# Performance work log

Hardware: AMD Instinct MI355X
Metric: run time of the kernel (lower is better)

The kernel has to match this reference:

```python
import jax, jax.numpy as jnp
import numpy as np

TAU = 2.0  # self.temperature
EPS = 1e-7

def setup_inputs() -> dict:
    key = jax.random.key(0)
    k1, k2, k3, k4, k5, k6 = jax.random.split(key, 6)
    B, S, H = 8, 4096, 512
    G, V, Dg = 2, 320, 128  # groups, codevectors per group, codevector_dim // G
    hidden_states = jax.random.normal(k1, (B, S, H), dtype=jnp.float32)
    mask_time_indices = jax.random.randint(k2, (B, S), 0, 2) > 0
    u = jax.random.uniform(k3, (B * S, G, V), dtype=jnp.float32, minval=1e-6, maxval=1.0 - 1e-6)
    gumbel_noise = -jnp.log(-jnp.log(u))  # standard Gumbel samples, as in F.gumbel_softmax
    W_proj = jax.random.normal(k4, (H, G * V), dtype=jnp.float32) * 0.02
    b_proj = jax.random.normal(k5, (G * V,), dtype=jnp.float32) * 0.02
    codevectors = jax.random.normal(k6, (G, V, Dg), dtype=jnp.float32)
    return {"hidden_states": hidden_states, "mask_time_indices": mask_time_indices,
            "gumbel_noise": gumbel_noise, "W_proj": W_proj, "b_proj": b_proj,
            "codevectors": codevectors}

def reference(hidden_states, mask_time_indices, gumbel_noise, W_proj, b_proj, codevectors):
    B, S, H = hidden_states.shape
    G, V, Dg = codevectors.shape
    N = B * S
    # weight projection: [B,S,H] -> [B,S,G*V] -> [N, G, V]
    logits = (jnp.einsum('bsh,hk->bsk', hidden_states, W_proj) + b_proj)
    logits = logits.reshape(N, G, V).astype(jnp.float32)
    # gumbel-softmax with hard=True (straight-through)
    y_soft = jax.nn.softmax((logits + gumbel_noise) / TAU, axis=-1)  # [N,G,V]
    idx = jnp.argmax(y_soft, axis=-1)                                 # [N,G]
    y_hard = jax.nn.one_hot(idx, V, dtype=y_soft.dtype)
    codevector_probs = y_hard + y_soft - jax.lax.stop_gradient(y_soft)
    # perplexity on the (noise-free) soft distribution, masked marginal
    soft_dist = jax.nn.softmax(logits, axis=-1)                       # [N,G,V]
    m = mask_time_indices.reshape(-1).astype(jnp.float32)             # [N]
    marginal = jnp.einsum('ngv,n->gv', soft_dist, m) / jnp.sum(m)
    perplexity = jnp.sum(jnp.exp(-jnp.sum(marginal * jnp.log(marginal + EPS), axis=-1)))
    # hard one-hot weighted sum over codebook == gather of selected codevector
    cv = jnp.einsum('ngv,gvd->ngd', codevector_probs, codevectors)    # [N,G,Dg]
    cv = cv.reshape(B, S, G * Dg)
    return cv, perplexity
```

## Files before the change

### kernel.cpp

```cpp
#include <hip/hip_runtime.h>
#include <hip/hip_bf16.h>
#include <math.h>

#define N_ROWS 32768
#define H      512
#define GV     640
#define V      320
#define DG     128
#define BM     64
#define NT     16

typedef __attribute__((ext_vector_type(4))) float f32x4;
typedef __attribute__((ext_vector_type(8))) short short8v;

static __device__ __forceinline__ short f2bf(float f) {
    unsigned int u = __float_as_uint(f);
    u += 0x7fffu + ((u >> 16) & 1u);
    return (short)(u >> 16);
}

__global__ __launch_bounds__(256)
void pack_w(const float* __restrict__ W, short* __restrict__ wp)
{
    int gid = blockIdx.x * 256 + threadIdx.x;
    int l   = gid & 63;
    int ct  = (gid >> 6) % 40;
    int t   = gid / (40 * 64);
    int row = t * 32 + 8 * (l >> 4);
    int col = ct * 16 + (l & 15);
    short8v pk;
    #pragma unroll
    for (int i = 0; i < 8; ++i)
        pk[i] = f2bf(W[(size_t)(row + i) * GV + col]);
    *(short8v*)(wp + (size_t)gid * 8) = pk;
}

__global__ __launch_bounds__(512, 2)
void gumbel_vq_main(const float* __restrict__ hidden,
                    const int*   __restrict__ mask,
                    const float* __restrict__ gumbel,
                    const short* __restrict__ wpack,
                    const float* __restrict__ bias,
                    const float* __restrict__ codevec,
                    float* __restrict__ out,
                    float* __restrict__ ws)
{
    __shared__ float smem[16 * 648];
    const int tid = threadIdx.x;
    const int tn  = tid & 63;
    const int wid = tid >> 6;
    const int wm  = wid >> 2, wn = wid & 3;
    const int q   = tn >> 4,  cn = tn & 15;
    const int row0 = blockIdx.x * BM;

    f32x4 acc[2][10];
    #pragma unroll
    for (int j = 0; j < 10; ++j) {
        float b = bias[wn * 160 + j * 16 + cn];
        f32x4 c; c[0] = b; c[1] = b; c[2] = b; c[3] = b;
        acc[0][j] = c; acc[1][j] = c;
    }

    const float* a0p = hidden + (size_t)(row0 + wm * 32 + cn) * H + 8 * q;
    const float* a1p = a0p + (size_t)16 * H;
    const short* bb  = wpack + ((size_t)(wn * 10) * 64 + tn) * 8;

    #pragma unroll 2
    for (int t = 0; t < NT; ++t) {
        float4 x00 = *(const float4*)(a0p + t * 32);
        float4 x01 = *(const float4*)(a0p + t * 32 + 4);
        float4 x10 = *(const float4*)(a1p + t * 32);
        float4 x11 = *(const float4*)(a1p + t * 32 + 4);
        short8v a0, a1;
        a0[0] = f2bf(x00.x); a0[1] = f2bf(x00.y); a0[2] = f2bf(x00.z); a0[3] = f2bf(x00.w);
        a0[4] = f2bf(x01.x); a0[5] = f2bf(x01.y); a0[6] = f2bf(x01.z); a0[7] = f2bf(x01.w);
        a1[0] = f2bf(x10.x); a1[1] = f2bf(x10.y); a1[2] = f2bf(x10.z); a1[3] = f2bf(x10.w);
        a1[4] = f2bf(x11.x); a1[5] = f2bf(x11.y); a1[6] = f2bf(x11.z); a1[7] = f2bf(x11.w);
        const short* bt = bb + t * 20480;
        #pragma unroll
        for (int j = 0; j < 10; ++j) {
            short8v bf = *(const short8v*)(bt + j * 512);
            acc[0][j] = __builtin_amdgcn_mfma_f32_16x16x32_bf16(a0, bf, acc[0][j], 0, 0, 0);
            acc[1][j] = __builtin_amdgcn_mfma_f32_16x16x32_bf16(a1, bf, acc[1][j], 0, 0, 0);
        }
    }

    const int cA = 4 * tn;
    const int cB = 256 + 4 * tn;
    const int cC = 512 + 2 * tn;
    const bool b_in1 = (tn >= 16);

    float marg[10];
    #pragma unroll
    for (int s = 0; s < 10; ++s) marg[s] = 0.f;

    #pragma unroll
    for (int c = 0; c < 4; ++c) {
        __syncthreads();
        if (wm == (c >> 1)) {
            const int rt = c & 1;
            #pragma unroll
            for (int j = 0; j < 10; ++j) {
                const int col = wn * 160 + j * 16 + cn;
                f32x4 v = acc[rt][j];
                #pragma unroll
                for (int r = 0; r < 4; ++r)
                    smem[(4 * q + r) * 648 + col] = v[r];
            }
        }
        __syncthreads();

        #pragma unroll
        for (int rr = 0; rr < 2; ++rr) {
            const int rl  = wid * 2 + rr;
            const int row = row0 + c * 16 + rl;
            const float mrow = (mask[row] != 0) ? 1.f : 0.f;

            const float* lrow = &smem[rl * 648];
            float4 aA = *(const float4*)(lrow + cA);
            float4 aB = *(const float4*)(lrow + cB);
            float2 aC = *(const float2*)(lrow + cC);
            const float* gr = gumbel + (size_t)row * GV;
            float4 gA = *(const float4*)(gr + cA);
            float4 gB = *(const float4*)(gr + cB);
            float2 gC = *(const float2*)(gr + cC);

            float l0 = aA.x, l1 = aA.y, l2 = aA.z, l3 = aA.w;
            float l4 = aB.x, l5 = aB.y, l6 = aB.z, l7 = aB.w;
            float l8 = aC.x, l9 = aC.y;

            float z0 = l0 + gA.x, z1 = l1 + gA.y, z2 = l2 + gA.z, z3 = l3 + gA.w;
            float zm0 = z0; int zi0 = cA;
            if (z1 > zm0) { zm0 = z1; zi0 = cA + 1; }
            if (z2 > zm0) { zm0 = z2; zi0 = cA + 2; }
            if (z3 > zm0) { zm0 = z3; zi0 = cA + 3; }
            float lm0 = fmaxf(fmaxf(l0, l1), fmaxf(l2, l3));
            float z8 = l8 + gC.x, z9 = l9 + gC.y;
            float zm1 = z8; int zi1 = cC;
            if (z9 > zm1) { zm1 = z9; zi1 = cC + 1; }
            float lm1 = fmaxf(l8, l9);
            {
                float z4 = l4 + gB.x, z5 = l5 + gB.y, z6 = l6 + gB.z, z7 = l7 + gB.w;
                float zmB = z4; int ziB = cB;
                if (z5 > zmB) { zmB = z5; ziB = cB + 1; }
                if (z6 > zmB) { zmB = z6; ziB = cB + 2; }
                if (z7 > zmB) { zmB = z7; ziB = cB + 3; }
                float lmB = fmaxf(fmaxf(l4, l5), fmaxf(l6, l7));
                if (!b_in1) {
                    if (zmB > zm0 || (zmB == zm0 && ziB < zi0)) { zm0 = zmB; zi0 = ziB; }
                    lm0 = fmaxf(lm0, lmB);
                } else {
                    if (zmB > zm1 || (zmB == zm1 && ziB < zi1)) { zm1 = zmB; zi1 = ziB; }
                    lm1 = fmaxf(lm1, lmB);
                }
            }

            #pragma unroll
            for (int d = 32; d >= 1; d >>= 1) {
                float oz; int oi;
                oz = __shfl_xor(zm0, d, 64); oi = __shfl_xor(zi0, d, 64);
                if (oz > zm0 || (oz == zm0 && oi < zi0)) { zm0 = oz; zi0 = oi; }
                oz = __shfl_xor(zm1, d, 64); oi = __shfl_xor(zi1, d, 64);
                if (oz > zm1 || (oz == zm1 && oi < zi1)) { zm1 = oz; zi1 = oi; }
                lm0 = fmaxf(lm0, __shfl_xor(lm0, d, 64));
                lm1 = fmaxf(lm1, __shfl_xor(lm1, d, 64));
            }

            float lmB = b_in1 ? lm1 : lm0;
            float p0 = __expf(l0 - lm0), p1 = __expf(l1 - lm0), p2 = __expf(l2 - lm0), p3 = __expf(l3 - lm0);
            float p4 = __expf(l4 - lmB), p5 = __expf(l5 - lmB), p6 = __expf(l6 - lmB), p7 = __expf(l7 - lmB);
            float p8 = __expf(l8 - lm1), p9 = __expf(l9 - lm1);
            float pB = p4 + p5 + p6 + p7;
            float s0 = p0 + p1 + p2 + p3 + (b_in1 ? 0.f : pB);
            float s1 = p8 + p9 + (b_in1 ? pB : 0.f);
            #pragma unroll
            for (int d = 32; d >= 1; d >>= 1) {
                s0 += __shfl_xor(s0, d, 64);
                s1 += __shfl_xor(s1, d, 64);
            }
            float inv0 = mrow / s0, inv1 = mrow / s1;
            float invB = b_in1 ? inv1 : inv0;
            marg[0] += p0 * inv0; marg[1] += p1 * inv0; marg[2] += p2 * inv0; marg[3] += p3 * inv0;
            marg[4] += p4 * invB; marg[5] += p5 * invB; marg[6] += p6 * invB; marg[7] += p7 * invB;
            marg[8] += p8 * inv1; marg[9] += p9 * inv1;

            int g   = tn >> 5;
            int idx = g ? (zi1 - V) : zi0;
            const float4* src = (const float4*)(codevec + ((size_t)g * V + idx) * DG);
            float4 vv = src[tn & 31];
            ((float4*)(out + (size_t)row * (2 * DG) + g * DG))[tn & 31] = vv;
        }
    }

    __syncthreads();
    float* mybuf = &smem[wid * GV];
    mybuf[cA] = marg[0]; mybuf[cA + 1] = marg[1]; mybuf[cA + 2] = marg[2]; mybuf[cA + 3] = marg[3];
    mybuf[cB] = marg[4]; mybuf[cB + 1] = marg[5]; mybuf[cB + 2] = marg[6]; mybuf[cB + 3] = marg[7];
    mybuf[cC] = marg[8]; mybuf[cC + 1] = marg[9];
    __syncthreads();
    for (int col = tid; col < GV; col += 512) {
        float s = 0.f;
        #pragma unroll
        for (int w = 0; w < 8; ++w) s += smem[w * GV + col];
        atomicAdd(&ws[col], s);
    }

    if (wid == 0) {
        int mr = (mask[row0 + tn] != 0);
        unsigned long long b = __ballot(mr);
        if (tn == 0) atomicAdd(&ws[GV], (float)__popcll(b));
    }
}

__global__ void gumbel_vq_finalize(const float* __restrict__ ws, float* __restrict__ out)
{
    __shared__ float red[GV];
    int t = threadIdx.x;
    float cnt = ws[GV];
    float p = ws[t] / cnt;
    red[t] = p * logf(p + 1e-7f);
    __syncthreads();
    if (t == 0) {
        float e0 = 0.f, e1 = 0.f;
        for (int i = 0; i < V; ++i)  e0 += red[i];
        for (int i = V; i < GV; ++i) e1 += red[i];
        out[(size_t)N_ROWS * 2 * DG] = expf(-e0) + expf(-e1);
    }
}

extern "C" void kernel_launch(void* const* d_in, const int* in_sizes, int n_in,
                              void* d_out, int out_size, void* d_ws, size_t ws_size,
                              hipStream_t stream)
{
    const float* hidden  = (const float*)d_in[0];
    const int*   mask    = (const int*)  d_in[1];
    const float* gumbel  = (const float*)d_in[2];
    const float* W       = (const float*)d_in[3];
    const float* bias    = (const float*)d_in[4];
    const float* codevec = (const float*)d_in[5];
    float* out = (float*)d_out;
    float* ws  = (float*)d_ws;
    short* wpack = (short*)((char*)d_ws + 4096);

    hipMemsetAsync(d_ws, 0, (GV + 1) * sizeof(float), stream);
    pack_w<<<160, 256, 0, stream>>>(W, wpack);
    gumbel_vq_main<<<N_ROWS / BM, 512, 0, stream>>>(hidden, mask, gumbel, wpack, bias, codevec, out, ws);
    gumbel_vq_finalize<<<1, GV, 0, stream>>>(ws, out);
}
```

Before: 110.5 us.

## Prepack hidden states to bf16 MFMA layout in output buffer, use 1024-thread blocks

Adds a pre-pass kernel that converts hidden states to bf16 and writes them in the MFMA fragment layout. It uses the output buffer as scratch, and each block's packed region lines up with the output rows that block later writes. The main kernel now loads prepacked A fragments directly instead of loading fp32 and converting inline. Blocks grow to 16 waves, each owning a single 16-row tile with 10 accumulators. That cuts register pressure and lets each wave post-process one row per stage. The cost is an extra full pass over the activations: the fp32 input is read once more and the bf16 copy is written and read back. Correctness also depends on the scratch aliasing staying block-local.

```diff
diff --git a/kernel.cpp b/kernel.cpp
--- a/kernel.cpp
+++ b/kernel.cpp
@@ -35,14 +35,30 @@
     *(short8v*)(wp + (size_t)gid * 8) = pk;
 }
 
-__global__ __launch_bounds__(512, 2)
-void gumbel_vq_main(const float* __restrict__ hidden,
+__global__ __launch_bounds__(256)
+void pack_a(const float* __restrict__ hidden, short* __restrict__ ap)
+{
+    int gid = blockIdx.x * 256 + threadIdx.x;
+    int l   = gid & 63;
+    int t   = (gid >> 6) & 15;
+    int rt  = gid >> 10;
+    const float* src = hidden + (size_t)(rt * 16 + (l & 15)) * H + t * 32 + 8 * (l >> 4);
+    float4 x0 = *(const float4*)src;
+    float4 x1 = *(const float4*)(src + 4);
+    short8v pk;
+    pk[0] = f2bf(x0.x); pk[1] = f2bf(x0.y); pk[2] = f2bf(x0.z); pk[3] = f2bf(x0.w);
+    pk[4] = f2bf(x1.x); pk[5] = f2bf(x1.y); pk[6] = f2bf(x1.z); pk[7] = f2bf(x1.w);
+    *(short8v*)(ap + (size_t)gid * 8) = pk;
+}
+
+__global__ __launch_bounds__(1024, 4)
+void gumbel_vq_main(const short* apack,
                     const int*   __restrict__ mask,
                     const float* __restrict__ gumbel,
                     const short* __restrict__ wpack,
                     const float* __restrict__ bias,
                     const float* __restrict__ codevec,
-                    float* __restrict__ out,
+                    float* out,
                     float* __restrict__ ws)
 {
     __shared__ float smem[16 * 648];
@@ -53,35 +69,24 @@
     const int q   = tn >> 4,  cn = tn & 15;
     const int row0 = blockIdx.x * BM;
 
-    f32x4 acc[2][10];
+    f32x4 acc[10];
     #pragma unroll
     for (int j = 0; j < 10; ++j) {
         float b = bias[wn * 160 + j * 16 + cn];
         f32x4 c; c[0] = b; c[1] = b; c[2] = b; c[3] = b;
-        acc[0][j] = c; acc[1][j] = c;
-    }
-
-    const float* a0p = hidden + (size_t)(row0 + wm * 32 + cn) * H + 8 * q;
-    const float* a1p = a0p + (size_t)16 * H;
-    const short* bb  = wpack + ((size_t)(wn * 10) * 64 + tn) * 8;
-
-    #pragma unroll 2
+        acc[j] = c;
+    }
+
+    const short* ab = apack + ((size_t)(blockIdx.x * 4 + wm) * NT * 64 + tn) * 8;
+    const short* bb = wpack + ((size_t)(wn * 10) * 64 + tn) * 8;
+
+    #pragma unroll
     for (int t = 0; t < NT; ++t) {
-        float4 x00 = *(const float4*)(a0p + t * 32);
-        float4 x01 = *(const float4*)(a0p + t * 32 + 4);
-        float4 x10 = *(const float4*)(a1p + t * 32);
-        float4 x11 = *(const float4*)(a1p + t * 32 + 4);
-        short8v a0, a1;
-        a0[0] = f2bf(x00.x); a0[1] = f2bf(x00.y); a0[2] = f2bf(x00.z); a0[3] = f2bf(x00.w);
-        a0[4] = f2bf(x01.x); a0[5] = f2bf(x01.y); a0[6] = f2bf(x01.z); a0[7] = f2bf(x01.w);
-        a1[0] = f2bf(x10.x); a1[1] = f2bf(x10.y); a1[2] = f2bf(x10.z); a1[3] = f2bf(x10.w);
-        a1[4] = f2bf(x11.x); a1[5] = f2bf(x11.y); a1[6] = f2bf(x11.z); a1[7] = f2bf(x11.w);
-        const short* bt = bb + t * 20480;
+        short8v a = *(const short8v*)(ab + (size_t)t * 512);
         #pragma unroll
         for (int j = 0; j < 10; ++j) {
-            short8v bf = *(const short8v*)(bt + j * 512);
-            acc[0][j] = __builtin_amdgcn_mfma_f32_16x16x32_bf16(a0, bf, acc[0][j], 0, 0, 0);
-            acc[1][j] = __builtin_amdgcn_mfma_f32_16x16x32_bf16(a1, bf, acc[1][j], 0, 0, 0);
+            short8v bf = *(const short8v*)(bb + (size_t)t * 20480 + j * 512);
+            acc[j] = __builtin_amdgcn_mfma_f32_16x16x32_bf16(a, bf, acc[j], 0, 0, 0);
         }
     }
 
@@ -97,12 +102,11 @@
     #pragma unroll
     for (int c = 0; c < 4; ++c) {
         __syncthreads();
-        if (wm == (c >> 1)) {
-            const int rt = c & 1;
+        if (wm == c) {
             #pragma unroll
             for (int j = 0; j < 10; ++j) {
                 const int col = wn * 160 + j * 16 + cn;
-                f32x4 v = acc[rt][j];
+                f32x4 v = acc[j];
                 #pragma unroll
                 for (int r = 0; r < 4; ++r)
                     smem[(4 * q + r) * 648 + col] = v[r];
@@ -110,86 +114,82 @@
         }
         __syncthreads();
 
-        #pragma unroll
-        for (int rr = 0; rr < 2; ++rr) {
-            const int rl  = wid * 2 + rr;
-            const int row = row0 + c * 16 + rl;
-            const float mrow = (mask[row] != 0) ? 1.f : 0.f;
-
-            const float* lrow = &smem[rl * 648];
-            float4 aA = *(const float4*)(lrow + cA);
-            float4 aB = *(const float4*)(lrow + cB);
-            float2 aC = *(const float2*)(lrow + cC);
-            const float* gr = gumbel + (size_t)row * GV;
-            float4 gA = *(const float4*)(gr + cA);
-            float4 gB = *(const float4*)(gr + cB);
-            float2 gC = *(const float2*)(gr + cC);
-
-            float l0 = aA.x, l1 = aA.y, l2 = aA.z, l3 = aA.w;
-            float l4 = aB.x, l5 = aB.y, l6 = aB.z, l7 = aB.w;
-            float l8 = aC.x, l9 = aC.y;
-
-            float z0 = l0 + gA.x, z1 = l1 + gA.y, z2 = l2 + gA.z, z3 = l3 + gA.w;
-            float zm0 = z0; int zi0 = cA;
-            if (z1 > zm0) { zm0 = z1; zi0 = cA + 1; }
-            if (z2 > zm0) { zm0 = z2; zi0 = cA + 2; }
-            if (z3 > zm0) { zm0 = z3; zi0 = cA + 3; }
-            float lm0 = fmaxf(fmaxf(l0, l1), fmaxf(l2, l3));
-            float z8 = l8 + gC.x, z9 = l9 + gC.y;
-            float zm1 = z8; int zi1 = cC;
-            if (z9 > zm1) { zm1 = z9; zi1 = cC + 1; }
-            float lm1 = fmaxf(l8, l9);
-            {
-                float z4 = l4 + gB.x, z5 = l5 + gB.y, z6 = l6 + gB.z, z7 = l7 + gB.w;
-                float zmB = z4; int ziB = cB;
-                if (z5 > zmB) { zmB = z5; ziB = cB + 1; }
-                if (z6 > zmB) { zmB = z6; ziB = cB + 2; }
-                if (z7 > zmB) { zmB = z7; ziB = cB + 3; }
-                float lmB = fmaxf(fmaxf(l4, l5), fmaxf(l6, l7));
-                if (!b_in1) {
-                    if (zmB > zm0 || (zmB == zm0 && ziB < zi0)) { zm0 = zmB; zi0 = ziB; }
-                    lm0 = fmaxf(lm0, lmB);
-                } else {
-                    if (zmB > zm1 || (zmB == zm1 && ziB < zi1)) { zm1 = zmB; zi1 = ziB; }
-                    lm1 = fmaxf(lm1, lmB);
-                }
+        const int row = row0 + c * 16 + wid;
+        const float mrow = (mask[row] != 0) ? 1.f : 0.f;
+
+        const float* lp = &smem[wid * 648];
+        float4 aA = *(const float4*)(lp + cA);
+        float4 aB = *(const float4*)(lp + cB);
+        float2 aC = *(const float2*)(lp + cC);
+        const float* gr = gumbel + (size_t)row * GV;
+        float4 gA = *(const float4*)(gr + cA);
+        float4 gB = *(const float4*)(gr + cB);
+        float2 gC = *(const float2*)(gr + cC);
+
+        float l0 = aA.x, l1 = aA.y, l2 = aA.z, l3 = aA.w;
+        float l4 = aB.x, l5 = aB.y, l6 = aB.z, l7 = aB.w;
+        float l8 = aC.x, l9 = aC.y;
+
+        float z0 = l0 + gA.x, z1 = l1 + gA.y, z2 = l2 + gA.z, z3 = l3 + gA.w;
+        float zm0 = z0; int zi0 = cA;
+        if (z1 > zm0) { zm0 = z1; zi0 = cA + 1; }
+        if (z2 > zm0) { zm0 = z2; zi0 = cA + 2; }
+        if (z3 > zm0) { zm0 = z3; zi0 = cA + 3; }
+        float lm0 = fmaxf(fmaxf(l0, l1), fmaxf(l2, l3));
+        float z8 = l8 + gC.x, z9 = l9 + gC.y;
+        float zm1 = z8; int zi1 = cC;
+        if (z9 > zm1) { zm1 = z9; zi1 = cC + 1; }
+        float lm1 = fmaxf(l8, l9);
+        {
+            float z4 = l4 + gB.x, z5 = l5 + gB.y, z6 = l6 + gB.z, z7 = l7 + gB.w;
+            float zmB = z4; int ziB = cB;
+            if (z5 > zmB) { zmB = z5; ziB = cB + 1; }
+            if (z6 > zmB) { zmB = z6; ziB = cB + 2; }
+            if (z7 > zmB) { zmB = z7; ziB = cB + 3; }
+            float lmB = fmaxf(fmaxf(l4, l5), fmaxf(l6, l7));
+            if (!b_in1) {
+                if (zmB > zm0 || (zmB == zm0 && ziB < zi0)) { zm0 = zmB; zi0 = ziB; }
+                lm0 = fmaxf(lm0, lmB);
+            } else {
+                if (zmB > zm1 || (zmB == zm1 && ziB < zi1)) { zm1 = zmB; zi1 = ziB; }
+                lm1 = fmaxf(lm1, lmB);
             }
-
-            #pragma unroll
-            for (int d = 32; d >= 1; d >>= 1) {
-                float oz; int oi;
-                oz = __shfl_xor(zm0, d, 64); oi = __shfl_xor(zi0, d, 64);
-                if (oz > zm0 || (oz == zm0 && oi < zi0)) { zm0 = oz; zi0 = oi; }
-                oz = __shfl_xor(zm1, d, 64); oi = __shfl_xor(zi1, d, 64);
-                if (oz > zm1 || (oz == zm1 && oi < zi1)) { zm1 = oz; zi1 = oi; }
-                lm0 = fmaxf(lm0, __shfl_xor(lm0, d, 64));
-                lm1 = fmaxf(lm1, __shfl_xor(lm1, d, 64));
-            }
-
-            float lmB = b_in1 ? lm1 : lm0;
-            float p0 = __expf(l0 - lm0), p1 = __expf(l1 - lm0), p2 = __expf(l2 - lm0), p3 = __expf(l3 - lm0);
-            float p4 = __expf(l4 - lmB), p5 = __expf(l5 - lmB), p6 = __expf(l6 - lmB), p7 = __expf(l7 - lmB);
-            float p8 = __expf(l8 - lm1), p9 = __expf(l9 - lm1);
-            float pB = p4 + p5 + p6 + p7;
-            float s0 = p0 + p1 + p2 + p3 + (b_in1 ? 0.f : pB);
-            float s1 = p8 + p9 + (b_in1 ? pB : 0.f);
-            #pragma unroll
-            for (int d = 32; d >= 1; d >>= 1) {
-                s0 += __shfl_xor(s0, d, 64);
-                s1 += __shfl_xor(s1, d, 64);
-            }
-            float inv0 = mrow / s0, inv1 = mrow / s1;
-            float invB = b_in1 ? inv1 : inv0;
-            marg[0] += p0 * inv0; marg[1] += p1 * inv0; marg[2] += p2 * inv0; marg[3] += p3 * inv0;
-            marg[4] += p4 * invB; marg[5] += p5 * invB; marg[6] += p6 * invB; marg[7] += p7 * invB;
-            marg[8] += p8 * inv1; marg[9] += p9 * inv1;
-
-            int g   = tn >> 5;
-            int idx = g ? (zi1 - V) : zi0;
-            const float4* src = (const float4*)(codevec + ((size_t)g * V + idx) * DG);
-            float4 vv = src[tn & 31];
-            ((float4*)(out + (size_t)row * (2 * DG) + g * DG))[tn & 31] = vv;
-        }
+        }
+
+        #pragma unroll
+        for (int d = 32; d >= 1; d >>= 1) {
+            float oz; int oi;
+            oz = __shfl_xor(zm0, d, 64); oi = __shfl_xor(zi0, d, 64);
+            if (oz > zm0 || (oz == zm0 && oi < zi0)) { zm0 = oz; zi0 = oi; }
+            oz = __shfl_xor(zm1, d, 64); oi = __shfl_xor(zi1, d, 64);
+            if (oz > zm1 || (oz == zm1 && oi < zi1)) { zm1 = oz; zi1 = oi; }
+            lm0 = fmaxf(lm0, __shfl_xor(lm0, d, 64));
+            lm1 = fmaxf(lm1, __shfl_xor(lm1, d, 64));
+        }
+
+        float lmB = b_in1 ? lm1 : lm0;
+        float p0 = __expf(l0 - lm0), p1 = __expf(l1 - lm0), p2 = __expf(l2 - lm0), p3 = __expf(l3 - lm0);
+        float p4 = __expf(l4 - lmB), p5 = __expf(l5 - lmB), p6 = __expf(l6 - lmB), p7 = __expf(l7 - lmB);
+        float p8 = __expf(l8 - lm1), p9 = __expf(l9 - lm1);
+        float pB = p4 + p5 + p6 + p7;
+        float s0 = p0 + p1 + p2 + p3 + (b_in1 ? 0.f : pB);
+        float s1 = p8 + p9 + (b_in1 ? pB : 0.f);
+        #pragma unroll
+        for (int d = 32; d >= 1; d >>= 1) {
+            s0 += __shfl_xor(s0, d, 64);
+            s1 += __shfl_xor(s1, d, 64);
+        }
+        float inv0 = mrow / s0, inv1 = mrow / s1;
+        float invB = b_in1 ? inv1 : inv0;
+        marg[0] += p0 * inv0; marg[1] += p1 * inv0; marg[2] += p2 * inv0; marg[3] += p3 * inv0;
+        marg[4] += p4 * invB; marg[5] += p5 * invB; marg[6] += p6 * invB; marg[7] += p7 * invB;
+        marg[8] += p8 * inv1; marg[9] += p9 * inv1;
+
+        int g   = tn >> 5;
+        int idx = g ? (zi1 - V) : zi0;
+        const float4* src = (const float4*)(codevec + ((size_t)g * V + idx) * DG);
+        float4 vv = src[tn & 31];
+        ((float4*)(out + (size_t)row * (2 * DG) + g * DG))[tn & 31] = vv;
     }
 
     __syncthreads();
@@ -198,11 +198,11 @@
     mybuf[cB] = marg[4]; mybuf[cB + 1] = marg[5]; mybuf[cB + 2] = marg[6]; mybuf[cB + 3] = marg[7];
     mybuf[cC] = marg[8]; mybuf[cC + 1] = marg[9];
     __syncthreads();
-    for (int col = tid; col < GV; col += 512) {
+    if (tid < GV) {
         float s = 0.f;
         #pragma unroll
-        for (int w = 0; w < 8; ++w) s += smem[w * GV + col];
-        atomicAdd(&ws[col], s);
+        for (int w = 0; w < 16; ++w) s += smem[w * GV + tid];
+        atomicAdd(&ws[tid], s);
     }
 
     if (wid == 0) {
@@ -241,9 +241,11 @@
     float* out = (float*)d_out;
     float* ws  = (float*)d_ws;
     short* wpack = (short*)((char*)d_ws + 4096);
+    short* apack = (short*)d_out;
 
     hipMemsetAsync(d_ws, 0, (GV + 1) * sizeof(float), stream);
     pack_w<<<160, 256, 0, stream>>>(W, wpack);
-    gumbel_vq_main<<<N_ROWS / BM, 512, 0, stream>>>(hidden, mask, gumbel, wpack, bias, codevec, out, ws);
+    pack_a<<<8192, 256, 0, stream>>>(hidden, apack);
+    gumbel_vq_main<<<N_ROWS / BM, 1024, 0, stream>>>(apack, mask, gumbel, wpack, bias, codevec, out, ws);
     gumbel_vq_finalize<<<1, GV, 0, stream>>>(ws, out);
 }
```

After: 119.4 us. +8.0%, slower.
